# Optimization experiments

Measured on AMD Instinct MI355X. Metric: run time of the kernel, lower is better.

## Reference

```python
import jax, jax.numpy as jnp
import numpy as np
from jax import lax

T_STEPS = 40
BATCH = 2048
UNITS = 1024
INPUT_DIM = 1024
Q_BASIS = 8
ORDER = 4  # skfda BSpline default (cubic)


def bspline_basis(ts, q, k=ORDER):
    """Cox-de Boor B-spline basis, n_basis=q, order k, domain [0,1]. ts: (T,) -> (T,q)."""
    ts = np.asarray(ts, dtype=np.float64)
    breaks = np.linspace(0.0, 1.0, q - k + 2)
    knots = np.concatenate([np.zeros(k - 1), breaks, np.ones(k - 1)])  # len q+k
    n0 = len(knots) - 1
    N = np.zeros((len(ts), n0))
    for i in range(n0):
        N[:, i] = ((ts >= knots[i]) & (ts < knots[i + 1])).astype(np.float64)
    for d in range(1, k):
        Nn = np.zeros((len(ts), n0 - d))
        for i in range(n0 - d):
            out = np.zeros(len(ts))
            den1 = knots[i + d] - knots[i]
            if den1 > 0:
                out += (ts - knots[i]) / den1 * N[:, i]
            den2 = knots[i + d + 1] - knots[i + 1]
            if den2 > 0:
                out += (knots[i + d + 1] - ts) / den2 * N[:, i + 1]
            Nn[:, i] = out
        N = Nn
    # at right endpoint t==1 only the last basis is nonzero (value 1)
    at_end = ts >= 1.0 - 1e-12
    N[at_end] = 0.0
    N[at_end, -1] = 1.0
    return N.astype(np.float32)


def setup_inputs() -> dict:
    key = jax.random.key(0)
    k1, k2, k3 = jax.random.split(key, 3)
    D = UNITS + INPUT_DIM
    x = jax.random.normal(k1, (BATCH, T_STEPS, INPUT_DIM), dtype=jnp.float32)
    h0 = jnp.zeros((BATCH, UNITS), dtype=jnp.float32)
    Qw = jax.random.normal(k2, (D, Q_BASIS * UNITS), dtype=jnp.float32) / np.sqrt(D)
    bias = jax.random.uniform(k3, (UNITS,), dtype=jnp.float32, minval=-0.05, maxval=0.05)
    Bt_all = jnp.asarray(bspline_basis(np.linspace(0.0, 1.0, T_STEPS), Q_BASIS))
    return {"x": x, "h0": h0, "Qw": Qw, "bias": bias, "Bt_all": Bt_all}


def reference(x, h0, Qw, bias, Bt_all):
    B, T, I = x.shape
    U = h0.shape[-1]
    q = Bt_all.shape[-1]
    D = Qw.shape[0]
    # block_diag(Bt,...,Bt).T contraction == reshape Q to (D, U, q) and contract q with Bt
    Qr = Qw.reshape(D, U, q)
    W_all = jnp.einsum('duq,tq->tdu', Qr, Bt_all)  # (T, D, U) per-step weight matrices

    def step(h, xw):
        x_t, W_t = xw                       # (B,I), (D,U)
        cat = jnp.concatenate([h, x_t], axis=-1)  # (B, U+I) = (B, D); state first, as in cell
        h_new = jnp.tanh(cat @ W_t + bias)
        return h_new, h_new

    xs = jnp.swapaxes(x, 0, 1)              # (T, B, I)
    _, hs = lax.scan(step, h0, (xs, W_all))
    return jnp.swapaxes(hs, 0, 1)           # (B, T, U)
```

## Files before the change

kernel.cpp:

```cpp
#include <hip/hip_runtime.h>
#include <hip/hip_fp16.h>

#define TS 40
#define NB 2048
#define NU 1024
#define NI 1024
#define ND 2048
#define UD (1024 * 2048)

typedef _Float16 half8 __attribute__((ext_vector_type(8)));
typedef _Float16 half4v __attribute__((ext_vector_type(4)));
typedef float floatx4 __attribute__((ext_vector_type(4)));

__device__ __forceinline__ float tanh_fast(float v) {
  float e = __expf(2.0f * v);
  return 1.0f - 2.0f / (e + 1.0f);
}

__device__ __forceinline__ void gload16(const void* g, void* l) {
  __builtin_amdgcn_global_load_lds(
      (const __attribute__((address_space(1))) void*)g,
      (__attribute__((address_space(3))) void*)l, 16, 0, 0);
}

__device__ __forceinline__ int tile_off(int r, int c8) {
  return (((((r >> 4) * 2 + (c8 >> 2)) << 6) + ((c8 & 3) << 4) + (r & 15)) << 4);
}


__global__ __launch_bounds__(256) void wprep(
    const float* __restrict__ Qw, const float* __restrict__ Bt,
    _Float16* __restrict__ W)
{
  __shared__ _Float16 ldsQ[64 * 512];
  __shared__ float ldsB[TS * 8];
  const int tid = threadIdx.x;
  const int kt = blockIdx.x;
  const int ut = blockIdx.y;
  for (int i = tid; i < TS * 8; i += 256) ldsB[i] = Bt[i];
  const float* qb = Qw + (size_t)(kt * 64) * 8192 + ut * 512;
#pragma unroll
  for (int i = 0; i < 32; ++i) {
    int s = i * 256 + tid;
    int dk = s >> 7, c4 = s & 127;
    float4 v = *(const float4*)(qb + (size_t)dk * 8192 + c4 * 4);
    _Float16* d = &ldsQ[dk * 512 + c4 * 4];
    d[0] = (_Float16)v.x; d[1] = (_Float16)v.y;
    d[2] = (_Float16)v.z; d[3] = (_Float16)v.w;
  }
  __syncthreads();
  const int w = tid >> 6, lane = tid & 63;
  const int dur = lane & 7, ko = lane >> 3;
#pragma unroll 1
  for (int sp = 0; sp < 2; ++sp) {
    const int stripe = w * 2 + sp;
    const int du = stripe * 8 + dur;
    float Q[8][8];
#pragma unroll
    for (int j = 0; j < 8; ++j)
#pragma unroll
      for (int q = 0; q < 8; ++q)
        Q[j][q] = (float)ldsQ[(ko * 8 + j) * 512 + du * 8 + q];
    const int obase = tile_off(du, ko);
#pragma unroll 1
    for (int t = 0; t < TS; ++t) {
      float b[8];
#pragma unroll
      for (int q = 0; q < 8; ++q) b[q] = ldsB[t * 8 + q];
      half8 v;
#pragma unroll
      for (int j = 0; j < 8; ++j) {
        float s = 0.f;
#pragma unroll
        for (int q = 0; q < 8; ++q) s += Q[j][q] * b[q];
        v[j] = (_Float16)s;
      }
      size_t tile = ((size_t)t * 16 + ut) * 32 + kt;
      *(half8*)((char*)W + tile * 8192 + obase) = v;
    }
  }
}

__global__ __launch_bounds__(256) void xprep(
    const float* __restrict__ x, _Float16* __restrict__ X)
{
  __shared__ char stage[8192];
  const int tid = threadIdx.x;
  const int bt = blockIdx.x, t = blockIdx.y;
  char* outb = (char*)X + ((size_t)(t * 32 + bt) * 16) * 8192;
  const int r = tid >> 2, cq = tid & 3;
#pragma unroll 1
  for (int kt = 0; kt < 16; ++kt) {
    const float* src =
        x + (size_t)(bt * 64 + r) * (TS * NI) + (size_t)t * NI + kt * 64 + cq * 16;
    float4 a0 = *(const float4*)(src);
    float4 a1 = *(const float4*)(src + 4);
    float4 a2 = *(const float4*)(src + 8);
    float4 a3 = *(const float4*)(src + 12);
    half8 h0, h1;
    h0[0] = (_Float16)a0.x; h0[1] = (_Float16)a0.y;
    h0[2] = (_Float16)a0.z; h0[3] = (_Float16)a0.w;
    h0[4] = (_Float16)a1.x; h0[5] = (_Float16)a1.y;
    h0[6] = (_Float16)a1.z; h0[7] = (_Float16)a1.w;
    h1[0] = (_Float16)a2.x; h1[1] = (_Float16)a2.y;
    h1[2] = (_Float16)a2.z; h1[3] = (_Float16)a2.w;
    h1[4] = (_Float16)a3.x; h1[5] = (_Float16)a3.y;
    h1[6] = (_Float16)a3.z; h1[7] = (_Float16)a3.w;
    *(half8*)(stage + tile_off(r, cq * 2)) = h0;
    *(half8*)(stage + tile_off(r, cq * 2 + 1)) = h1;
    __syncthreads();
    uint4 v0 = *(const uint4*)(stage + tid * 32);
    uint4 v1 = *(const uint4*)(stage + tid * 32 + 16);
    *(uint4*)(outb + (size_t)kt * 8192 + tid * 32) = v0;
    *(uint4*)(outb + (size_t)kt * 8192 + tid * 32 + 16) = v1;
    __syncthreads();
  }
}

__global__ __launch_bounds__(256) void hinit(const float* __restrict__ h0,
                                             _Float16* __restrict__ hb) {
  int g = blockIdx.x * 256 + threadIdx.x;
  int tile_id = g >> 9, rc = g & 511;
  int bt = tile_id >> 4, kt = tile_id & 15;
  int r = rc >> 3, c8 = rc & 7;
  const float* src = h0 + (size_t)(bt * 64 + r) * NU + kt * 64 + c8 * 8;
  float4 v0 = *(const float4*)src;
  float4 v1 = *(const float4*)(src + 4);
  half8 h;
  h[0] = (_Float16)v0.x; h[1] = (_Float16)v0.y;
  h[2] = (_Float16)v0.z; h[3] = (_Float16)v0.w;
  h[4] = (_Float16)v1.x; h[5] = (_Float16)v1.y;
  h[6] = (_Float16)v1.z; h[7] = (_Float16)v1.w;
  *(half8*)((char*)hb + (size_t)tile_id * 8192 + tile_off(r, c8)) = h;
}

__global__ __launch_bounds__(256) void xproj3(
    const _Float16* __restrict__ X, const _Float16* __restrict__ W,
    const float* __restrict__ bias, _Float16* __restrict__ pre)
{
  __shared__ char lds[65536];
  const int tid = threadIdx.x;
  const int bt2 = blockIdx.x;
  const int ut2 = blockIdx.y;
  const int t   = blockIdx.z;
  const int lane = tid & 63, w = tid >> 6;
  const int wm2 = w >> 1, wn2 = w & 1;
  const int l15 = lane & 15, lk = lane >> 4;

  const char* Xb = (const char*)X + (((size_t)t * 32 + bt2 * 2) * 16) * 8192;
  const char* Wb = (const char*)W + (((size_t)t * 16 + ut2 * 2) * 32 + 16) * 8192;

  float bv[4];
#pragma unroll
  for (int nf = 0; nf < 4; ++nf)
    bv[nf] = bias[ut2 * 128 + wn2 * 64 + nf * 16 + l15];

  auto issue = [&](int p) {
    const char* src = (w < 2)
        ? Xb + (size_t)w * (16 * 8192) + (size_t)p * 8192
        : Wb + (size_t)(w - 2) * (32 * 8192) + (size_t)p * 8192;
    src += lane * 16;
    char* dst = lds + (p & 1) * 32768 + w * 8192;
#pragma unroll
    for (int i = 0; i < 8; ++i) gload16(src + i * 1024, dst + i * 1024);
  };

  floatx4 acc[4][4] = {};

  auto comp = [&](int p) {
    const char* pA = lds + (p & 1) * 32768 + wm2 * 8192;
    const char* pB = lds + (p & 1) * 32768 + 16384 + wn2 * 8192;
    __builtin_amdgcn_s_setprio(1);
#pragma unroll
    for (int kk = 0; kk < 2; ++kk) {
      half8 af[4], bf[4];
#pragma unroll
      for (int mf = 0; mf < 4; ++mf)
        af[mf] = *(const half8*)(pA + ((mf * 2 + kk) << 10) + lane * 16);
#pragma unroll
      for (int nf = 0; nf < 4; ++nf)
        bf[nf] = *(const half8*)(pB + ((nf * 2 + kk) << 10) + lane * 16);
#pragma unroll
      for (int mf = 0; mf < 4; ++mf)
#pragma unroll
        for (int nf = 0; nf < 4; ++nf)
          acc[mf][nf] = __builtin_amdgcn_mfma_f32_16x16x32_f16(
              af[mf], bf[nf], acc[mf][nf], 0, 0, 0);
    }
    __builtin_amdgcn_s_setprio(0);
  };

  issue(0);
#pragma unroll 1
  for (int p = 0; p < 16; ++p) {
    if (p + 1 < 16) {
      issue(p + 1);
      asm volatile("s_waitcnt vmcnt(8)" ::: "memory");
    } else {
      asm volatile("s_waitcnt vmcnt(0)" ::: "memory");
    }
    __builtin_amdgcn_s_barrier();
    comp(p);
    __builtin_amdgcn_s_barrier();
  }

  __syncthreads();
#pragma unroll
  for (int mf = 0; mf < 4; ++mf)
#pragma unroll
    for (int nf = 0; nf < 4; ++nf)
#pragma unroll
      for (int j = 0; j < 4; ++j) {
        int bl = mf * 16 + (lk << 2) + j;
        int ul = nf * 16 + l15;
        int c8 = ul >> 3;
        int off = (wm2 * 2 + wn2) * 8192 + tile_off(bl, c8) + (ul & 7) * 2;
        *(_Float16*)(lds + off) = (_Float16)(acc[mf][nf][j] + bv[nf]);
      }
  __syncthreads();
#pragma unroll
  for (int q4 = 0; q4 < 4; ++q4) {
    int tb = q4 >> 1, tu = q4 & 1;
    char* gdst = (char*)pre +
        (((size_t)t * 32 + bt2 * 2 + tb) * 16 + ut2 * 2 + tu) * 8192;
#pragma unroll
    for (int i = 0; i < 2; ++i) {
      uint4 v = *(const uint4*)(lds + q4 * 8192 + i * 4096 + tid * 16);
      *(uint4*)(gdst + (size_t)i * 4096 + tid * 16) = v;
    }
  }
}

__global__ __launch_bounds__(256) void serial3(
    const _Float16* __restrict__ Wh,
    const _Float16* __restrict__ pret,
    const _Float16* __restrict__ hprev,
    _Float16* __restrict__ hnext,
    float* __restrict__ outt)
{
  __shared__ uint4 lds4[4608];
  const int tid = threadIdx.x, bid = blockIdx.x;
  const int bt = bid & 31, ut = bid >> 5;
  const int lane = tid & 63, w = tid >> 6;
  const int wm = w >> 1, wn = w & 1;
  const int l15 = lane & 15, lk = lane >> 4;
  const int b0 = bt * 64, u0 = ut * 64;

  {
    const char* src = (const char*)pret + ((size_t)(bt * 16 + ut)) * 8192 +
                      w * 2048 + lane * 16;
    char* dst = (char*)(lds4 + 4096) + w * 2048;
    gload16(src, dst);
    gload16(src + 1024, dst + 1024);
  }

  const char* Hb = (const char*)hprev + (size_t)bt * 16 * 8192;
  const char* Wb = (const char*)Wh + (size_t)ut * 32 * 8192;

  auto issue = [&](int kt) {
    char* la = (char*)lds4 + (kt & 3) * 16384 + w * 2048;
    const char* ga = Hb + (size_t)kt * 8192 + w * 2048 + lane * 16;
    const char* gb = Wb + (size_t)kt * 8192 + w * 2048 + lane * 16;
    gload16(ga, la);
    gload16(ga + 1024, la + 1024);
    gload16(gb, la + 8192);
    gload16(gb + 1024, la + 8192 + 1024);
  };

  floatx4 acc[2][2] = {};

  issue(0);
  issue(1);
  issue(2);
#pragma unroll 1
  for (int p = 0; p < 16; ++p) {
    if (p < 14)       asm volatile("s_waitcnt vmcnt(8)" ::: "memory");
    else if (p == 14) asm volatile("s_waitcnt vmcnt(4)" ::: "memory");
    else              asm volatile("s_waitcnt vmcnt(0)" ::: "memory");
    __builtin_amdgcn_s_barrier();
    if (p + 3 < 16) issue(p + 3);
    const char* pA = (const char*)lds4 + (p & 3) * 16384;
    const char* pB = pA + 8192;
    __builtin_amdgcn_s_setprio(1);
#pragma unroll
    for (int kk = 0; kk < 2; ++kk) {
      half8 af[2], bf[2];
#pragma unroll
      for (int mf = 0; mf < 2; ++mf)
        af[mf] = *(const half8*)(pA + ((((wm * 2 + mf) * 2 + kk) << 10) + lane * 16));
#pragma unroll
      for (int nf = 0; nf < 2; ++nf)
        bf[nf] = *(const half8*)(pB + ((((wn * 2 + nf) * 2 + kk) << 10) + lane * 16));
#pragma unroll
      for (int mf = 0; mf < 2; ++mf)
#pragma unroll
        for (int nf = 0; nf < 2; ++nf)
          acc[mf][nf] = __builtin_amdgcn_mfma_f32_16x16x32_f16(
              af[mf], bf[nf], acc[mf][nf], 0, 0, 0);
    }
    __builtin_amdgcn_s_setprio(0);
  }

  __syncthreads();
  const char* pl = (const char*)(lds4 + 4096);
#pragma unroll
  for (int mf = 0; mf < 2; ++mf)
#pragma unroll
    for (int nf = 0; nf < 2; ++nf)
#pragma unroll
      for (int j = 0; j < 4; ++j) {
        int bl = wm * 32 + mf * 16 + (lk << 2) + j;
        int ul = wn * 32 + nf * 16 + l15;
        int c8 = ul >> 3;
        int off = tile_off(bl, c8) + (ul & 7) * 2;
        float pv = (float)*(const _Float16*)(pl + off);
        float v = tanh_fast(acc[mf][nf][j] + pv);
        outt[(size_t)(b0 + bl) * (TS * NU) + u0 + ul] = v;
        *(_Float16*)((char*)lds4 + off) = (_Float16)v;
      }
  __syncthreads();
  {
    char* gdst = (char*)hnext + ((size_t)(bt * 16 + ut)) * 8192;
    uint4 v0 = *((const uint4*)lds4 + tid * 2);
    uint4 v1 = *((const uint4*)lds4 + tid * 2 + 1);
    *(uint4*)(gdst + (size_t)tid * 32) = v0;
    *(uint4*)(gdst + (size_t)tid * 32 + 16) = v1;
  }
}

__global__ __launch_bounds__(256) void wprep_lin(
    const float* __restrict__ Qw, const float* __restrict__ Bt,
    _Float16* __restrict__ W, int t0, int nt)
{
  __shared__ float ldsQ[32 * 257];
  __shared__ float ldsB[TS * 8];
  const int tid = threadIdx.x;
  const int k0 = blockIdx.x * 32;
  const int u0 = blockIdx.y * 32;
  for (int i = tid; i < TS * 8; i += 256) ldsB[i] = Bt[i];
  const float* qbase = Qw + (size_t)k0 * 8192 + (size_t)u0 * 8;
#pragma unroll
  for (int i = 0; i < 8; ++i) {
    int s = i * 256 + tid;
    int r = s >> 6, c4 = s & 63;
    float4 v = *(const float4*)(qbase + (size_t)r * 8192 + c4 * 4);
    float* d = &ldsQ[r * 257 + c4 * 4];
    d[0] = v.x; d[1] = v.y; d[2] = v.z; d[3] = v.w;
  }
  __syncthreads();
  const int kl = tid & 31;
  const int ug = tid >> 5;
#pragma unroll
  for (int p = 0; p < 4; ++p) {
    int uu = p * 8 + ug;
    float q[8];
#pragma unroll
    for (int j = 0; j < 8; ++j) q[j] = ldsQ[kl * 257 + uu * 8 + j];
    size_t obase = (size_t)(u0 + uu) * 2048 + k0 + kl;
    for (int tt = 0; tt < nt; ++tt) {
      const float* bt = &ldsB[(t0 + tt) * 8];
      float v = 0.f;
#pragma unroll
      for (int j = 0; j < 8; ++j) v += q[j] * bt[j];
      W[(size_t)tt * UD + obase] = (_Float16)v;
    }
  }
}

__global__ __launch_bounds__(256) void step_gemm(
    const float* __restrict__ xt, const float* __restrict__ hp, long hstride,
    const _Float16* __restrict__ Wt, const float* __restrict__ bias,
    float* __restrict__ outt)
{
  __shared__ _Float16 ldsA[2][64 * 64];
  __shared__ _Float16 ldsB[2][128 * 64];
  const int tid = threadIdx.x;
  const int b0 = blockIdx.x * 64;
  const int u0 = blockIdx.y * 128;
  const int lane = tid & 63;
  const int wv = tid >> 6;
  const int wm = wv >> 1, wn = wv & 1;
  const int l15 = lane & 15, lk = lane >> 4;

  float4 areg[4];
  uint4 breg[4];

  auto stage_load = [&](int kt) {
    const int k0 = kt * 64;
    const float* src; size_t stride; int koff;
    if (k0 < NU) { src = hp; stride = (size_t)hstride; koff = k0; }
    else { src = xt; stride = (size_t)TS * NI; koff = k0 - NU; }
#pragma unroll
    for (int i = 0; i < 4; ++i) {
      int s = i * 256 + tid;
      int r = s >> 4, c4 = s & 15;
      areg[i] = *(const float4*)(src + (size_t)(b0 + r) * stride + koff + c4 * 4);
    }
    const _Float16* wsrc = Wt + (size_t)u0 * 2048 + k0;
#pragma unroll
    for (int i = 0; i < 4; ++i) {
      int s = i * 256 + tid;
      int u = s >> 3, c8 = s & 7;
      breg[i] = *(const uint4*)(wsrc + (size_t)u * 2048 + c8 * 8);
    }
  };

  auto stage_write = [&](int buf) {
    char* pA = (char*)&ldsA[buf][0];
    char* pB = (char*)&ldsB[buf][0];
#pragma unroll
    for (int i = 0; i < 4; ++i) {
      int s = i * 256 + tid;
      int r = s >> 4, c4 = s & 15;
      half4v h;
      h[0] = (_Float16)areg[i].x; h[1] = (_Float16)areg[i].y;
      h[2] = (_Float16)areg[i].z; h[3] = (_Float16)areg[i].w;
      int off = (r * 128 + c4 * 8) ^ ((r & 7) << 4);
      *(half4v*)(pA + off) = h;
    }
#pragma unroll
    for (int i = 0; i < 4; ++i) {
      int s = i * 256 + tid;
      int u = s >> 3, c8 = s & 7;
      int off = (u * 128 + c8 * 16) ^ ((u & 7) << 4);
      *(uint4*)(pB + off) = breg[i];
    }
  };

  floatx4 acc[2][4] = {};

  auto compute = [&](int buf) {
    const char* pA = (const char*)&ldsA[buf][0];
    const char* pB = (const char*)&ldsB[buf][0];
#pragma unroll
    for (int kk = 0; kk < 2; ++kk) {
      half8 af[2], bf[4];
#pragma unroll
      for (int mf = 0; mf < 2; ++mf) {
        int r = wm * 32 + mf * 16 + l15;
        int off = r * 128 + ((((kk << 2) | lk) ^ (r & 7)) << 4);
        af[mf] = *(const half8*)(pA + off);
      }
#pragma unroll
      for (int nf = 0; nf < 4; ++nf) {
        int u = wn * 64 + nf * 16 + l15;
        int off = u * 128 + ((((kk << 2) | lk) ^ (u & 7)) << 4);
        bf[nf] = *(const half8*)(pB + off);
      }
#pragma unroll
      for (int mf = 0; mf < 2; ++mf)
#pragma unroll
        for (int nf = 0; nf < 4; ++nf)
          acc[mf][nf] =
              __builtin_amdgcn_mfma_f32_16x16x32_f16(af[mf], bf[nf], acc[mf][nf], 0, 0, 0);
    }
  };

  stage_load(0);
  stage_write(0);
  __syncthreads();
#pragma unroll 1
  for (int kt = 0; kt < 32; ++kt) {
    int cur = kt & 1;
    if (kt + 1 < 32) stage_load(kt + 1);
    compute(cur);
    if (kt + 1 < 32) stage_write(cur ^ 1);
    __syncthreads();
  }

#pragma unroll
  for (int mf = 0; mf < 2; ++mf)
#pragma unroll
    for (int nf = 0; nf < 4; ++nf) {
      int u = u0 + wn * 64 + nf * 16 + l15;
      float bv = bias[u];
      int brow = b0 + wm * 32 + mf * 16 + (lk << 2);
#pragma unroll
      for (int j = 0; j < 4; ++j) {
        float prev = acc[mf][nf][j] + bv;
        outt[(size_t)(brow + j) * (TS * NU) + u] = tanh_fast(prev);
      }
    }
}

extern "C" void kernel_launch(void* const* d_in, const int* in_sizes, int n_in,
                              void* d_out, int out_size, void* d_ws, size_t ws_size,
                              hipStream_t stream) {
  const float* x    = (const float*)d_in[0];
  const float* h0   = (const float*)d_in[1];
  const float* Qw   = (const float*)d_in[2];
  const float* bias = (const float*)d_in[3];
  const float* Bt   = (const float*)d_in[4];
  float* out = (float*)d_out;

  char* ws = (char*)d_ws;
  const size_t w_bytes    = (size_t)UD * TS * sizeof(_Float16);
  const size_t x_bytes    = w_bytes;
  const size_t pre_bytes  = w_bytes;
  const size_t slot_bytes = (size_t)NB * NU * sizeof(_Float16);
  const size_t need = w_bytes + x_bytes + pre_bytes + 2 * slot_bytes;

  if (ws_size >= need) {
    _Float16* W   = (_Float16*)ws;
    _Float16* X   = (_Float16*)(ws + w_bytes);
    _Float16* pre = (_Float16*)(ws + w_bytes + x_bytes);
    _Float16* hb  = (_Float16*)(ws + w_bytes + x_bytes + pre_bytes);
    const size_t SLOT = (size_t)NB * NU;

    wprep<<<dim3(32, 16), 256, 0, stream>>>(Qw, Bt, W);
    xprep<<<dim3(32, 40), 256, 0, stream>>>(x, X);
    hinit<<<dim3(1024), 256, 0, stream>>>(h0, hb);
    xproj3<<<dim3(16, 8, TS), 256, 0, stream>>>(X, W, bias, pre);

    for (int t = 0; t < TS; ++t) {
      const _Float16* hprev = hb + (size_t)(t & 1) * SLOT;
      _Float16* hnext = hb + (size_t)((t + 1) & 1) * SLOT;
      serial3<<<dim3(512), 256, 0, stream>>>(
          W + (size_t)t * UD, pre + (size_t)t * SLOT, hprev, hnext,
          out + (size_t)t * NU);
    }
  } else {
    _Float16* W = (_Float16*)ws;
    const bool big = ws_size >= w_bytes;
    if (big) wprep_lin<<<dim3(64, 32), 256, 0, stream>>>(Qw, Bt, W, 0, TS);
    for (int t = 0; t < TS; ++t) {
      const _Float16* Wtp;
      if (big) {
        Wtp = W + (size_t)t * UD;
      } else {
        wprep_lin<<<dim3(64, 32), 256, 0, stream>>>(Qw, Bt, W, t, 1);
        Wtp = W;
      }
      const float* hp = (t == 0) ? h0 : out + (size_t)(t - 1) * NU;
      long hstride = (t == 0) ? NU : (long)TS * NU;
      step_gemm<<<dim3(32, 8), 256, 0, stream>>>(
          x + (size_t)t * NI, hp, hstride, Wtp, bias, out + (size_t)t * NU);
    }
  }
}
```

Baseline: 1.002 ms.

## Store projection output in per-thread fragment layout and remap serial blocks by XCD

Measured after the change: 968.9 us. 1.03x faster.

```diff
diff --git a/kernel.cpp b/kernel.cpp
--- a/kernel.cpp
+++ b/kernel.cpp
@@ -134,7 +134,7 @@
   *(half8*)((char*)hb + (size_t)tile_id * 8192 + tile_off(r, c8)) = h;
 }
 
-__global__ __launch_bounds__(256) void xproj3(
+__global__ __launch_bounds__(256) void xproj4(
     const _Float16* __restrict__ X, const _Float16* __restrict__ W,
     const float* __restrict__ bias, _Float16* __restrict__ pre)
 {
@@ -204,54 +204,52 @@
     __builtin_amdgcn_s_barrier();
   }
 
-  __syncthreads();
-#pragma unroll
-  for (int mf = 0; mf < 4; ++mf)
-#pragma unroll
-    for (int nf = 0; nf < 4; ++nf)
-#pragma unroll
-      for (int j = 0; j < 4; ++j) {
-        int bl = mf * 16 + (lk << 2) + j;
-        int ul = nf * 16 + l15;
-        int c8 = ul >> 3;
-        int off = (wm2 * 2 + wn2) * 8192 + tile_off(bl, c8) + (ul & 7) * 2;
-        *(_Float16*)(lds + off) = (_Float16)(acc[mf][nf][j] + bv[nf]);
-      }
-  __syncthreads();
-#pragma unroll
-  for (int q4 = 0; q4 < 4; ++q4) {
-    int tb = q4 >> 1, tu = q4 & 1;
-    char* gdst = (char*)pre +
-        (((size_t)t * 32 + bt2 * 2 + tb) * 16 + ut2 * 2 + tu) * 8192;
-#pragma unroll
-    for (int i = 0; i < 2; ++i) {
-      uint4 v = *(const uint4*)(lds + q4 * 8192 + i * 4096 + tid * 16);
-      *(uint4*)(gdst + (size_t)i * 4096 + tid * 16) = v;
-    }
-  }
-}
-
-__global__ __launch_bounds__(256) void serial3(
+  char* pbase = (char*)pre + (size_t)t * (512 * 8192);
+#pragma unroll
+  for (int ws_ = 0; ws_ < 4; ++ws_) {
+    int wmS = ws_ >> 1, wnS = ws_ & 1;
+    _Float16 hv[16];
+#pragma unroll
+    for (int mfl = 0; mfl < 2; ++mfl)
+#pragma unroll
+      for (int nfl = 0; nfl < 2; ++nfl) {
+        int mfp = wmS * 2 + mfl, nfp = wnS * 2 + nfl;
+#pragma unroll
+        for (int j = 0; j < 4; ++j)
+          hv[((mfl * 2 + nfl) << 2) + j] = (_Float16)(acc[mfp][nfp][j] + bv[nfp]);
+      }
+    int bidS = (bt2 * 2 + wm2) + 32 * (ut2 * 2 + wn2);
+    int tidS = ws_ * 64 + lane;
+    char* dst = pbase + ((size_t)bidS * 256 + tidS) * 32;
+    *(uint4*)dst = ((const uint4*)hv)[0];
+    *(uint4*)(dst + 16) = ((const uint4*)hv)[1];
+  }
+}
+
+__global__ __launch_bounds__(256) void serial4(
     const _Float16* __restrict__ Wh,
     const _Float16* __restrict__ pret,
     const _Float16* __restrict__ hprev,
     _Float16* __restrict__ hnext,
     float* __restrict__ outt)
 {
-  __shared__ uint4 lds4[4608];
+  __shared__ uint4 lds4[4096];
   const int tid = threadIdx.x, bid = blockIdx.x;
-  const int bt = bid & 31, ut = bid >> 5;
+  const int xcd = bid & 7, kblk = bid >> 3;
+  const int bt = (xcd & 3) * 8 + (kblk & 7);
+  const int ut = (xcd >> 2) * 8 + (kblk >> 3);
+  const int bidS = bt + 32 * ut;
   const int lane = tid & 63, w = tid >> 6;
   const int wm = w >> 1, wn = w & 1;
   const int l15 = lane & 15, lk = lane >> 4;
   const int b0 = bt * 64, u0 = ut * 64;
 
+  uint4 prv0, prv1;
   {
-    const char* src = (const char*)pret + ((size_t)(bt * 16 + ut)) * 8192 +
-                      w * 2048 + lane * 16;
-    char* dst = (char*)(lds4 + 4096) + w * 2048;
-    gload16(src, dst);
-    gload16(src + 1024, dst + 1024);
+    const uint4* pp = (const uint4*)((const char*)pret +
+                                     ((size_t)bidS * 256 + tid) * 32);
+    prv0 = pp[0];
+    prv1 = pp[1];
   }
 
   const char* Hb = (const char*)hprev + (size_t)bt * 16 * 8192;
@@ -301,31 +299,27 @@
     __builtin_amdgcn_s_setprio(0);
   }
 
-  __syncthreads();
-  const char* pl = (const char*)(lds4 + 4096);
+  const _Float16* pr = (const _Float16*)&prv0;
+  _Float16 prh[16];
+  *(uint4*)&prh[0] = prv0;
+  *(uint4*)&prh[8] = prv1;
 #pragma unroll
   for (int mf = 0; mf < 2; ++mf)
 #pragma unroll
-    for (int nf = 0; nf < 2; ++nf)
+    for (int nf = 0; nf < 2; ++nf) {
+      int u = u0 + wn * 32 + nf * 16 + l15;
+      int brow = b0 + wm * 32 + mf * 16 + (lk << 2);
 #pragma unroll
       for (int j = 0; j < 4; ++j) {
-        int bl = wm * 32 + mf * 16 + (lk << 2) + j;
-        int ul = wn * 32 + nf * 16 + l15;
-        int c8 = ul >> 3;
-        int off = tile_off(bl, c8) + (ul & 7) * 2;
-        float pv = (float)*(const _Float16*)(pl + off);
-        float v = tanh_fast(acc[mf][nf][j] + pv);
-        outt[(size_t)(b0 + bl) * (TS * NU) + u0 + ul] = v;
-        *(_Float16*)((char*)lds4 + off) = (_Float16)v;
-      }
-  __syncthreads();
-  {
-    char* gdst = (char*)hnext + ((size_t)(bt * 16 + ut)) * 8192;
-    uint4 v0 = *((const uint4*)lds4 + tid * 2);
-    uint4 v1 = *((const uint4*)lds4 + tid * 2 + 1);
-    *(uint4*)(gdst + (size_t)tid * 32) = v0;
-    *(uint4*)(gdst + (size_t)tid * 32 + 16) = v1;
-  }
+        int b = brow + j;
+        float p = (float)prh[((mf * 2 + nf) << 2) + j];
+        float v = tanh_fast(acc[mf][nf][j] + p);
+        outt[(size_t)b * (TS * NU) + u] = v;
+        *(_Float16*)((char*)hnext + (((size_t)(bt * 16 + ut)) << 13) +
+                     tile_off(b & 63, (u & 63) >> 3) + (u & 7) * 2) = (_Float16)v;
+      }
+    }
+  (void)pr;
 }
 
 __global__ __launch_bounds__(256) void wprep_lin(
@@ -510,12 +504,12 @@
     wprep<<<dim3(32, 16), 256, 0, stream>>>(Qw, Bt, W);
     xprep<<<dim3(32, 40), 256, 0, stream>>>(x, X);
     hinit<<<dim3(1024), 256, 0, stream>>>(h0, hb);
-    xproj3<<<dim3(16, 8, TS), 256, 0, stream>>>(X, W, bias, pre);
+    xproj4<<<dim3(16, 8, TS), 256, 0, stream>>>(X, W, bias, pre);
 
     for (int t = 0; t < TS; ++t) {
       const _Float16* hprev = hb + (size_t)(t & 1) * SLOT;
       _Float16* hnext = hb + (size_t)((t + 1) & 1) * SLOT;
-      serial3<<<dim3(512), 256, 0, stream>>>(
+      serial4<<<dim3(512), 256, 0, stream>>>(
           W + (size_t)t * UD, pre + (size_t)t * SLOT, hprev, hnext,
           out + (size_t)t * NU);
     }
```
